# Optimization experiments

Measured on AMD Instinct MI355X. Metric: run time of the kernel, lower is better.

Reference implementation:

```python
import jax, jax.numpy as jnp
import numpy as np

N_EMBED = 1024
NUM_EXPERTS = 8
TOP_K = 2
D_FF = 4 * N_EMBED
B, S = 4, 2048


def setup_inputs() -> dict:
    key = jax.random.key(0)
    ks = jax.random.split(key, 8)
    s = 0.02
    return {
        "x": jax.random.normal(ks[0], (B, S, N_EMBED), jnp.float32),
        "noise": jax.random.normal(ks[1], (B, S, NUM_EXPERTS), jnp.float32),
        "w_route": jax.random.normal(ks[2], (N_EMBED, NUM_EXPERTS), jnp.float32) * s,
        "b_route": jnp.zeros((NUM_EXPERTS,), jnp.float32),
        "w_noise": jax.random.normal(ks[3], (N_EMBED, NUM_EXPERTS), jnp.float32) * s,
        "b_noise": jnp.zeros((NUM_EXPERTS,), jnp.float32),
        "w1": jax.random.normal(ks[4], (NUM_EXPERTS, N_EMBED, D_FF), jnp.float32) * s,
        "b1": jnp.zeros((NUM_EXPERTS, D_FF), jnp.float32),
        "w2": jax.random.normal(ks[5], (NUM_EXPERTS, D_FF, N_EMBED), jnp.float32) * s,
        "b2": jnp.zeros((NUM_EXPERTS, N_EMBED), jnp.float32),
    }


def reference(x, noise, w_route, b_route, w_noise, b_noise, w1, b1, w2, b2):
    # NoisyTopkRouter: logits + N(0,1)*softplus(noise_logits), top-k, softmax
    # over a sparse (-inf filled) logit matrix -> gates are exactly 0 for
    # non-selected experts.
    logits = x @ w_route + b_route                                   # [B,S,E]
    noise_logits = x @ w_noise + b_noise                             # [B,S,E]
    noisy = logits + noise * jax.nn.softplus(noise_logits)           # [B,S,E]
    _, topi = jax.lax.top_k(noisy, TOP_K)                            # [B,S,k]
    sel = jax.nn.one_hot(topi, NUM_EXPERTS, dtype=bool).any(-2)      # [B,S,E]
    sparse_logits = jnp.where(sel, noisy, -jnp.inf)
    gates = jax.nn.softmax(sparse_logits, axis=-1)                   # [B,S,E]

    T = x.shape[0] * x.shape[1]
    xf = x.reshape(T, N_EMBED)                                       # [T,d]
    gf = gates.reshape(T, NUM_EXPERTS)                               # [T,E]

    # Dense per-expert MLP weighted by gates; gate==0 for unselected tokens,
    # so this matches the masked gather/scatter of the original exactly.
    out = jnp.zeros_like(xf)
    for e in range(NUM_EXPERTS):
        h = jax.nn.relu(xf @ w1[e] + b1[e])                          # [T,4d]
        y = h @ w2[e] + b2[e]                                        # [T,d]
        out = out + y * gf[:, e:e + 1]
    return out.reshape(x.shape)
```

## Files before the change

### kernel.cpp

```cpp
#include <hip/hip_runtime.h>

typedef __bf16 bf16_t;
typedef __bf16 bf16x8 __attribute__((ext_vector_type(8)));
typedef __bf16 bf16x4 __attribute__((ext_vector_type(4)));
typedef __bf16 bf16x2 __attribute__((ext_vector_type(2)));
typedef float  f32x4  __attribute__((ext_vector_type(4)));
typedef unsigned int u32;
typedef u32 u32x4 __attribute__((ext_vector_type(4)));

#define T_TOK 8192
#define DIM   1024
#define DFF   4096
#define NEXP  8

__device__ __forceinline__ void gll16(const void* g, void* l) {
    __builtin_amdgcn_global_load_lds(
        (const __attribute__((address_space(1))) char*)g,
        (__attribute__((address_space(3))) char*)l, 16, 0, 0);
}

__device__ __forceinline__ void transpose_tile(
    const float* __restrict__ src, bf16_t* __restrict__ dst,
    int R, int C, int r0, int c0, int tid, u32* lds)
{
    {
        int cg = tid & 15, rp = tid >> 4;
#pragma unroll
        for (int i = 0; i < 2; ++i) {
            int p = rp + i * 16;
            f32x4 a = *(const f32x4*)&src[(size_t)(r0 + 2 * p) * C + c0 + cg * 4];
            f32x4 b = *(const f32x4*)&src[(size_t)(r0 + 2 * p + 1) * C + c0 + cg * 4];
#pragma unroll
            for (int j = 0; j < 4; ++j) {
                int c = cg * 4 + j;
                union { bf16x2 h; u32 w; } cv;
                cv.h[0] = (bf16_t)a[j];
                cv.h[1] = (bf16_t)b[j];
                int ps = p ^ (((c >> 2) & 7) << 2);
                lds[c * 32 + ps] = cv.w;
            }
        }
    }
    __syncthreads();
    {
        int q = tid & 7, ccb = tid >> 3;
#pragma unroll
        for (int i = 0; i < 2; ++i) {
            int cc = ccb + i * 32;
            int ps = (q * 4) ^ ((((cc) >> 2) & 7) << 2);
            u32x4 v = *(const u32x4*)&lds[cc * 32 + ps];
            *(u32x4*)&dst[(size_t)(c0 + cc) * R + r0 + q * 8] = v;
        }
    }
}

__global__ __launch_bounds__(256) void fused_pre_kernel(
    const float* __restrict__ x, const float* __restrict__ noise,
    const float* __restrict__ w_route, const float* __restrict__ b_route,
    const float* __restrict__ w_noise, const float* __restrict__ b_noise,
    const float* __restrict__ w1, const float* __restrict__ w2,
    bf16_t* __restrict__ w1t, bf16_t* __restrict__ w2t, bf16_t* __restrict__ xb,
    int* __restrict__ counts, int* __restrict__ lists, float* __restrict__ gate_tok,
    int* __restrict__ inv)
{
    __shared__ u32 lds[64 * 32];
    int id = blockIdx.x;
    int tid = threadIdx.x;

    if (id >= 4096) {
        if (id < 12288) {
            int t1 = id - 4096;
            int e = t1 >> 10, rem = t1 & 1023;
            int bx = rem & 63, by = rem >> 6;
            transpose_tile(w1 + (size_t)e * DIM * DFF, w1t + (size_t)e * DIM * DFF,
                           DIM, DFF, by * 64, bx * 64, tid, lds);
        } else {
            int t2 = id - 12288;
            int e = t2 >> 10, rem = t2 & 1023;
            int bx = rem & 15, by = rem >> 4;
            transpose_tile(w2 + (size_t)e * DFF * DIM, w2t + (size_t)e * DFF * DIM,
                           DFF, DIM, by * 64, bx * 64, tid, lds);
        }
        return;
    }

    int wave = tid >> 6;
    int lane = tid & 63;

    if (id >= 2048) {
        int tok = (id - 2048) * 4 + wave;
        const f32x4* src = (const f32x4*)(x + (size_t)tok * DIM);
        bf16x8* dst = (bf16x8*)(xb + (size_t)tok * DIM);
#pragma unroll
        for (int j = 0; j < 2; ++j) {
            int c = lane + j * 64;
            f32x4 a = src[c * 2 + 0];
            f32x4 b = src[c * 2 + 1];
            bf16x8 o;
            o[0] = (bf16_t)a[0]; o[1] = (bf16_t)a[1]; o[2] = (bf16_t)a[2]; o[3] = (bf16_t)a[3];
            o[4] = (bf16_t)b[0]; o[5] = (bf16_t)b[1]; o[6] = (bf16_t)b[2]; o[7] = (bf16_t)b[3];
            dst[c] = o;
        }
        return;
    }

    int tok = id * 4 + wave;
    if (tok >= T_TOK) return;

    const float* xr = x + (size_t)tok * DIM;
    double aR[NEXP], aN[NEXP];
#pragma unroll
    for (int e = 0; e < NEXP; ++e) { aR[e] = 0.0; aN[e] = 0.0; }

#pragma unroll 4
    for (int i = 0; i < 16; ++i) {
        int k = lane + i * 64;
        double xv = (double)xr[k];
        const float4* wr4 = (const float4*)(w_route + (size_t)k * 8);
        const float4* wn4 = (const float4*)(w_noise + (size_t)k * 8);
        float4 r0 = wr4[0], r1 = wr4[1];
        float4 n0 = wn4[0], n1 = wn4[1];
        aR[0] += xv * (double)r0.x; aR[1] += xv * (double)r0.y;
        aR[2] += xv * (double)r0.z; aR[3] += xv * (double)r0.w;
        aR[4] += xv * (double)r1.x; aR[5] += xv * (double)r1.y;
        aR[6] += xv * (double)r1.z; aR[7] += xv * (double)r1.w;
        aN[0] += xv * (double)n0.x; aN[1] += xv * (double)n0.y;
        aN[2] += xv * (double)n0.z; aN[3] += xv * (double)n0.w;
        aN[4] += xv * (double)n1.x; aN[5] += xv * (double)n1.y;
        aN[6] += xv * (double)n1.z; aN[7] += xv * (double)n1.w;
    }
#pragma unroll
    for (int e = 0; e < NEXP; ++e) {
        for (int s = 1; s < 64; s <<= 1) {
            aR[e] += __shfl_xor(aR[e], s);
            aN[e] += __shfl_xor(aN[e], s);
        }
    }
    if (lane == 0) {
        double nv[NEXP];
#pragma unroll
        for (int e = 0; e < NEXP; ++e) {
            double lg = aR[e] + (double)b_route[e];
            double nl = aN[e] + (double)b_noise[e];
            double sp = (nl > 30.0) ? nl : log1p(exp(nl));
            nv[e] = lg + (double)noise[(size_t)tok * 8 + e] * sp;
        }
        int i1 = 0;
#pragma unroll
        for (int e = 1; e < NEXP; ++e) if (nv[e] > nv[i1]) i1 = e;
        int i2 = (i1 == 0) ? 1 : 0;
#pragma unroll
        for (int e = 0; e < NEXP; ++e) if (e != i1 && nv[e] > nv[i2]) i2 = e;
        double m = nv[i1];
        double e2 = exp(nv[i2] - m);
        double s = 1.0 + e2;
        gate_tok[2 * tok + 0] = (float)(1.0 / s);
        gate_tok[2 * tok + 1] = (float)(e2 / s);
        int p1 = atomicAdd(&counts[i1], 1);
        lists[i1 * T_TOK + p1] = 2 * tok + 0;
        inv[2 * tok + 0] = (i1 << 13) | p1;
        int p2 = atomicAdd(&counts[i2], 1);
        lists[i2 * T_TOK + p2] = 2 * tok + 1;
        inv[2 * tok + 1] = (i2 << 13) | p2;
    }
}

template<int K, int MODE>
__global__ __launch_bounds__(256) void moe_gemm_kernel(
    const bf16_t* __restrict__ Asrc, const bf16_t* __restrict__ Wt,
    const float* __restrict__ bias,
    const int* __restrict__ counts, const int* __restrict__ lists,
    const float* __restrict__ gate_tok,
    bf16_t* __restrict__ Hout, bf16_t* __restrict__ Yp)
{
    constexpr int N = (MODE == 0) ? DFF : DIM;
    constexpr int NT = K / 64;
    constexpr int NY = N / 128;

    int wg = blockIdx.x + 64 * (blockIdx.y + NY * blockIdx.z);
    int e = wg & 7;
    int inner = wg >> 3;
    int xi = inner & 63;
    int yi = inner >> 6;

    int cnt, base;
    {
        int s = 0, c = 0, b = 0;
#pragma unroll
        for (int i = 0; i < NEXP; ++i) {
            int ci = counts[i];
            if (i == e) { b = s; c = ci; }
            s += ci;
        }
        cnt = c; base = b;
    }
    int m0 = xi * 128;
    if (m0 >= cnt) return;
    int n0 = yi * 128;
    const int* list = lists + e * T_TOK;
    const bf16_t* W = Wt + (size_t)e * N * K;

    __shared__ __attribute__((aligned(16))) bf16_t Ah0[128 * 64];
    __shared__ __attribute__((aligned(16))) bf16_t Bh0[128 * 64];
    __shared__ __attribute__((aligned(16))) bf16_t Ah1[128 * 64];
    __shared__ __attribute__((aligned(16))) bf16_t Bh1[128 * 64];

    int tid = threadIdx.x;
    int lane = tid & 63;
    int wave = tid >> 6;
    int wr = wave >> 1, wc = wave & 1;

    int kcs = (((lane & 7) ^ (lane >> 3)) << 3);
    const bf16_t* pA[4];
    const bf16_t* pB[4];
#pragma unroll
    for (int i = 0; i < 4; ++i) {
        int c = wave * 4 + i;
        int r = c * 8 + (lane >> 3);
        int ridx = m0 + r; if (ridx > cnt - 1) ridx = cnt - 1;
        size_t arow;
        if constexpr (MODE == 0) arow = (size_t)(list[ridx] >> 1);
        else                     arow = (size_t)(base + ridx);
        pA[i] = Asrc + arow * K + kcs;
        pB[i] = W + (size_t)(n0 + r) * K + kcs;
    }

    f32x4 acc[4][4];
#pragma unroll
    for (int m = 0; m < 4; ++m)
#pragma unroll
        for (int n = 0; n < 4; ++n)
            acc[m][n] = (f32x4){0.f, 0.f, 0.f, 0.f};

    int g = lane >> 4, ln15 = lane & 15, ln7 = lane & 7;

#define STAGE(An, Bn, k0) do {                                               \
    _Pragma("unroll") for (int i = 0; i < 4; ++i) {                          \
        int c = wave * 4 + i;                                                \
        gll16(pA[i] + (k0), (An) + c * 512);                                 \
        gll16(pB[i] + (k0), (Bn) + c * 512);                                 \
    } } while (0)

#define COMPUTE(Ab, Bb) do {                                                 \
    _Pragma("unroll") for (int kk = 0; kk < 2; ++kk) {                       \
        bf16x8 a[4], b[4];                                                   \
        int sw = (((kk * 4 + g) ^ ln7) << 3);                                \
        _Pragma("unroll") for (int n = 0; n < 4; ++n)                        \
            b[n] = *(const bf16x8*)((Bb) + (wc * 64 + n * 16 + ln15) * 64 + sw); \
        _Pragma("unroll") for (int m = 0; m < 4; ++m)                        \
            a[m] = *(const bf16x8*)((Ab) + (wr * 64 + m * 16 + ln15) * 64 + sw); \
        __builtin_amdgcn_s_setprio(1);                                       \
        _Pragma("unroll") for (int m = 0; m < 4; ++m)                        \
            _Pragma("unroll") for (int n = 0; n < 4; ++n)                    \
                acc[m][n] = __builtin_amdgcn_mfma_f32_16x16x32_bf16(a[m], b[n], acc[m][n], 0, 0, 0); \
        __builtin_amdgcn_s_setprio(0);                                       \
    } } while (0)

#define FENCE() __builtin_amdgcn_sched_barrier(0)
#define WAITV(n) asm volatile("s_waitcnt vmcnt(" #n ")" ::: "memory")

    STAGE(Ah0, Bh0, 0);

    for (int kt = 0; kt < NT; kt += 2) {
        if (kt + 1 < NT) { STAGE(Ah1, Bh1, (kt + 1) * 64); WAITV(8); }
        else             { WAITV(0); }
        FENCE(); __builtin_amdgcn_s_barrier(); FENCE();
        COMPUTE(Ah0, Bh0);
        FENCE(); __builtin_amdgcn_s_barrier(); FENCE();
        if (kt + 2 < NT) { STAGE(Ah0, Bh0, (kt + 2) * 64); WAITV(8); }
        else             { WAITV(0); }
        FENCE(); __builtin_amdgcn_s_barrier(); FENCE();
        COMPUTE(Ah1, Bh1);
        FENCE(); __builtin_amdgcn_s_barrier(); FENCE();
    }
#undef STAGE
#undef COMPUTE
#undef FENCE
#undef WAITV

    int l4 = lane >> 4;
    float bs[4];
#pragma unroll
    for (int n = 0; n < 4; ++n)
        bs[n] = bias[e * N + n0 + wc * 64 + n * 16 + ln15];
#pragma unroll
    for (int m = 0; m < 4; ++m) {
#pragma unroll
        for (int j = 0; j < 4; ++j) {
            int grow = m0 + wr * 64 + m * 16 + l4 * 4 + j;
            if (grow >= cnt) continue;
            if constexpr (MODE == 0) {
#pragma unroll
                for (int n = 0; n < 4; ++n) {
                    int gcol = n0 + wc * 64 + n * 16 + ln15;
                    float v = acc[m][n][j] + bs[n];
                    Hout[(size_t)(base + grow) * DFF + gcol] = (bf16_t)fmaxf(v, 0.f);
                }
            } else {
                float gt = gate_tok[list[grow]];
#pragma unroll
                for (int n = 0; n < 4; ++n) {
                    int gcol = n0 + wc * 64 + n * 16 + ln15;
                    Yp[(size_t)(base + grow) * DIM + gcol] = (bf16_t)(gt * (acc[m][n][j] + bs[n]));
                }
            }
        }
    }
}

__global__ __launch_bounds__(256) void combine_kernel(
    const bf16_t* __restrict__ Yp, const int* __restrict__ inv,
    const int* __restrict__ counts, float* __restrict__ out)
{
    int bs[NEXP];
    {
        int s = 0;
#pragma unroll
        for (int i = 0; i < NEXP; ++i) { bs[i] = s; s += counts[i]; }
    }
    int q = threadIdx.x >> 7, i = threadIdx.x & 127;
    int t = blockIdx.x * 2 + q;
    int v0 = inv[2 * t], v1 = inv[2 * t + 1];
    int p0 = bs[v0 >> 13] + (v0 & 8191);
    int p1 = bs[v1 >> 13] + (v1 & 8191);
    bf16x8 va = ((const bf16x8*)(Yp + (size_t)p0 * DIM))[i];
    bf16x8 vb = ((const bf16x8*)(Yp + (size_t)p1 * DIM))[i];
    f32x4 o0, o1;
#pragma unroll
    for (int j = 0; j < 4; ++j) {
        o0[j] = (float)va[j] + (float)vb[j];
        o1[j] = (float)va[4 + j] + (float)vb[4 + j];
    }
    f32x4* o = (f32x4*)(out + (size_t)t * DIM + i * 8);
    o[0] = o0;
    o[1] = o1;
}

extern "C" void kernel_launch(void* const* d_in, const int* in_sizes, int n_in,
                              void* d_out, int out_size, void* d_ws, size_t ws_size,
                              hipStream_t stream) {
    const float* x       = (const float*)d_in[0];
    const float* noise   = (const float*)d_in[1];
    const float* w_route = (const float*)d_in[2];
    const float* b_route = (const float*)d_in[3];
    const float* w_noise = (const float*)d_in[4];
    const float* b_noise = (const float*)d_in[5];
    const float* w1      = (const float*)d_in[6];
    const float* b1      = (const float*)d_in[7];
    const float* w2      = (const float*)d_in[8];
    const float* b2      = (const float*)d_in[9];
    float* out = (float*)d_out;

    char* ws = (char*)d_ws;
    size_t off = 0;
    auto alloc = [&](size_t bytes) {
        off = (off + 255) & ~(size_t)255;
        size_t r = off; off += bytes; return r;
    };
    int*    counts   = (int*)   (ws + alloc(32));
    int*    lists    = (int*)   (ws + alloc((size_t)NEXP * T_TOK * 4));
    float*  gate_tok = (float*) (ws + alloc((size_t)T_TOK * 2 * 4));
    int*    inv      = (int*)   (ws + alloc((size_t)T_TOK * 2 * 4));
    bf16_t* w1t      = (bf16_t*)(ws + alloc((size_t)NEXP * DFF * DIM * 2));
    bf16_t* w2t      = (bf16_t*)(ws + alloc((size_t)NEXP * DIM * DFF * 2));
    bf16_t* xb       = (bf16_t*)(ws + alloc((size_t)T_TOK * DIM * 2));
    bf16_t* H        = (bf16_t*)(ws + alloc((size_t)T_TOK * 2 * DFF * 2));
    bf16_t* Yp       = w1t;
    (void)ws_size; (void)in_sizes; (void)n_in; (void)out_size;

    hipMemsetAsync(counts, 0, 32, stream);

    fused_pre_kernel<<<20480, 256, 0, stream>>>(x, noise, w_route, b_route, w_noise, b_noise,
                                                w1, w2, w1t, w2t, xb, counts, lists, gate_tok, inv);

    moe_gemm_kernel<DIM, 0><<<dim3(64, DFF / 128, NEXP), 256, 0, stream>>>(
        xb, w1t, b1, counts, lists, gate_tok, H, nullptr);
    moe_gemm_kernel<DFF, 1><<<dim3(64, DIM / 128, NEXP), 256, 0, stream>>>(
        H, w2t, b2, counts, lists, gate_tok, nullptr, Yp);

    combine_kernel<<<T_TOK / 2, 256, 0, stream>>>(Yp, inv, counts, out);
}
```

Baseline: 737.3 us.

## Move w2 transpose from pre-kernel into first expert GEMM launch

The fp32-to-bf16 transpose of w2 moves out of the preprocessing kernel and becomes extra blocks appended to the first expert GEMM grid, which is flattened to a 1D launch. The aim is to overlap this memory-bound transpose with the compute-bound GEMM1 blocks, including those that exit early for idle tiles, rather than serialising it before routing completes. The risk is that transpose blocks compete with GEMM blocks for bandwidth and CUs. They are scheduled last, so they could end up as a tail after GEMM1.

Result: faster. 698.1 us (-5.3%).

```diff
diff --git a/kernel.cpp b/kernel.cpp
--- a/kernel.cpp
+++ b/kernel.cpp
@@ -58,8 +58,8 @@
     const float* __restrict__ x, const float* __restrict__ noise,
     const float* __restrict__ w_route, const float* __restrict__ b_route,
     const float* __restrict__ w_noise, const float* __restrict__ b_noise,
-    const float* __restrict__ w1, const float* __restrict__ w2,
-    bf16_t* __restrict__ w1t, bf16_t* __restrict__ w2t, bf16_t* __restrict__ xb,
+    const float* __restrict__ w1,
+    bf16_t* __restrict__ w1t, bf16_t* __restrict__ xb,
     int* __restrict__ counts, int* __restrict__ lists, float* __restrict__ gate_tok,
     int* __restrict__ inv)
 {
@@ -68,19 +68,11 @@
     int tid = threadIdx.x;
 
     if (id >= 4096) {
-        if (id < 12288) {
-            int t1 = id - 4096;
-            int e = t1 >> 10, rem = t1 & 1023;
-            int bx = rem & 63, by = rem >> 6;
-            transpose_tile(w1 + (size_t)e * DIM * DFF, w1t + (size_t)e * DIM * DFF,
-                           DIM, DFF, by * 64, bx * 64, tid, lds);
-        } else {
-            int t2 = id - 12288;
-            int e = t2 >> 10, rem = t2 & 1023;
-            int bx = rem & 15, by = rem >> 4;
-            transpose_tile(w2 + (size_t)e * DFF * DIM, w2t + (size_t)e * DFF * DIM,
-                           DFF, DIM, by * 64, bx * 64, tid, lds);
-        }
+        int t1 = id - 4096;
+        int e = t1 >> 10, rem = t1 & 1023;
+        int bx = rem & 63, by = rem >> 6;
+        transpose_tile(w1 + (size_t)e * DIM * DFF, w1t + (size_t)e * DIM * DFF,
+                       DIM, DFF, by * 64, bx * 64, tid, lds);
         return;
     }
 
@@ -171,13 +163,33 @@
     const float* __restrict__ bias,
     const int* __restrict__ counts, const int* __restrict__ lists,
     const float* __restrict__ gate_tok,
-    bf16_t* __restrict__ Hout, bf16_t* __restrict__ Yp)
+    bf16_t* __restrict__ Hout, bf16_t* __restrict__ Yp,
+    const float* __restrict__ w2src, bf16_t* __restrict__ w2t)
 {
     constexpr int N = (MODE == 0) ? DFF : DIM;
     constexpr int NT = K / 64;
     constexpr int NY = N / 128;
 
-    int wg = blockIdx.x + 64 * (blockIdx.y + NY * blockIdx.z);
+    __shared__ __attribute__((aligned(16))) bf16_t Ah0[128 * 64];
+    __shared__ __attribute__((aligned(16))) bf16_t Bh0[128 * 64];
+    __shared__ __attribute__((aligned(16))) bf16_t Ah1[128 * 64];
+    __shared__ __attribute__((aligned(16))) bf16_t Bh1[128 * 64];
+
+    int wg;
+    if constexpr (MODE == 0) {
+        wg = blockIdx.x;
+        if (wg >= 16384) {
+            int t2 = wg - 16384;
+            int e = t2 >> 10, rem = t2 & 1023;
+            int bx = rem & 15, by = rem >> 4;
+            transpose_tile(w2src + (size_t)e * DFF * DIM, w2t + (size_t)e * DFF * DIM,
+                           DFF, DIM, by * 64, bx * 64, threadIdx.x, (u32*)Ah0);
+            return;
+        }
+    } else {
+        wg = blockIdx.x + 64 * (blockIdx.y + NY * blockIdx.z);
+    }
+
     int e = wg & 7;
     int inner = wg >> 3;
     int xi = inner & 63;
@@ -199,11 +211,6 @@
     int n0 = yi * 128;
     const int* list = lists + e * T_TOK;
     const bf16_t* W = Wt + (size_t)e * N * K;
-
-    __shared__ __attribute__((aligned(16))) bf16_t Ah0[128 * 64];
-    __shared__ __attribute__((aligned(16))) bf16_t Bh0[128 * 64];
-    __shared__ __attribute__((aligned(16))) bf16_t Ah1[128 * 64];
-    __shared__ __attribute__((aligned(16))) bf16_t Bh1[128 * 64];
 
     int tid = threadIdx.x;
     int lane = tid & 63;
@@ -370,13 +377,13 @@
 
     hipMemsetAsync(counts, 0, 32, stream);
 
-    fused_pre_kernel<<<20480, 256, 0, stream>>>(x, noise, w_route, b_route, w_noise, b_noise,
-                                                w1, w2, w1t, w2t, xb, counts, lists, gate_tok, inv);
-
-    moe_gemm_kernel<DIM, 0><<<dim3(64, DFF / 128, NEXP), 256, 0, stream>>>(
-        xb, w1t, b1, counts, lists, gate_tok, H, nullptr);
+    fused_pre_kernel<<<12288, 256, 0, stream>>>(x, noise, w_route, b_route, w_noise, b_noise,
+                                                w1, w1t, xb, counts, lists, gate_tok, inv);
+
+    moe_gemm_kernel<DIM, 0><<<24576, 256, 0, stream>>>(
+        xb, w1t, b1, counts, lists, gate_tok, H, nullptr, w2, w2t);
     moe_gemm_kernel<DFF, 1><<<dim3(64, DIM / 128, NEXP), 256, 0, stream>>>(
-        H, w2t, b2, counts, lists, gate_tok, nullptr, Yp);
+        H, w2t, b2, counts, lists, gate_tok, nullptr, Yp, nullptr, nullptr);
 
     combine_kernel<<<T_TOK / 2, 256, 0, stream>>>(Yp, inv, counts, out);
 }
```
